# Optimization experiments

Hardware: AMD Instinct MI355X
Metric: run time of the kernel (lower is better)

## Reference

```python
import jax, jax.numpy as jnp
import numpy as np

B, N, K, OUT = 32, 8192, 64, 384
EPS = 1e-5  # BatchNorm eps (torch default)


def setup_inputs() -> dict:
    key = jax.random.key(0)
    ks = jax.random.split(key, 20)
    p = lambda k, shape: jax.random.normal(k, shape, dtype=jnp.float32) * 0.05
    return {
        "normalized_xyz": jax.random.normal(ks[0], (B, N, 3), dtype=jnp.float32),
        "choice": jax.random.randint(ks[1], (B, N), 0, K, dtype=jnp.int32),
        # first_conv: Conv1d(3,128,1) + BN(128) + ReLU + Conv1d(128,256,1)
        "W1": p(ks[2], (128, 3)), "b1": p(ks[3], (128,)),
        "g1": 1.0 + p(ks[4], (128,)), "be1": p(ks[5], (128,)),
        "m1": p(ks[6], (128,)),
        "v1": jax.random.uniform(ks[7], (128,), minval=0.5, maxval=1.5, dtype=jnp.float32),
        "W2": p(ks[8], (256, 128)), "b2": p(ks[9], (256,)),
        # second_conv: Conv1d(512,512,1) + BN(512) + ReLU + Conv1d(512,OUT,1)
        "W3": p(ks[10], (512, 512)), "b3": p(ks[11], (512,)),
        "g2": 1.0 + p(ks[12], (512,)), "be2": p(ks[13], (512,)),
        "m2": p(ks[14], (512,)),
        "v2": jax.random.uniform(ks[15], (512,), minval=0.5, maxval=1.5, dtype=jnp.float32),
        "W4": p(ks[16], (OUT, 512)), "b4": p(ks[17], (OUT,)),
    }


def reference(normalized_xyz, choice, W1, b1, g1, be1, m1, v1, W2, b2,
              W3, b3, g2, be2, m2, v2, W4, b4):
    Bsz, Np, _ = normalized_xyz.shape
    # first_conv: 1x1 convs == per-point matmuls (channel-last layout)
    h = jnp.einsum('bnc,dc->bnd', normalized_xyz, W1) + b1          # [B,N,128]
    h = g1 * (h - m1) / jnp.sqrt(v1 + EPS) + be1                    # BN (eval)
    h = jax.nn.relu(h)
    feat = jnp.einsum('bnd,ed->bne', h, W2) + b2                    # [B,N,256]
    # segmented max over clusters: offset segment ids per batch element
    seg = (choice + jnp.arange(Bsz, dtype=choice.dtype)[:, None] * K).reshape(-1)
    fg = jax.ops.segment_max(feat.reshape(Bsz * Np, -1), seg,
                             num_segments=Bsz * K).reshape(Bsz, K, -1)  # [B,K,256]
    # gather cluster max back to each point
    fg_pts = jnp.take_along_axis(fg, choice[:, :, None], axis=1)   # [B,N,256]
    h = jnp.concatenate([fg_pts, feat], axis=-1)                    # [B,N,512]
    # second_conv
    h = jnp.einsum('bnc,dc->bnd', h, W3) + b3                       # [B,N,512]
    h = g2 * (h - m2) / jnp.sqrt(v2 + EPS) + be2
    h = jax.nn.relu(h)
    feat2 = jnp.einsum('bnd,ed->bne', h, W4) + b4                   # [B,N,OUT]
    out = jax.ops.segment_max(feat2.reshape(Bsz * Np, -1), seg,
                              num_segments=Bsz * K).reshape(Bsz, K, -1)  # [B,K,OUT]
    return out
```

## Files before the change

kernel.cpp:

```cpp
#include <hip/hip_runtime.h>
#include <hip/hip_bf16.h>

#define BB 32
#define NN 8192
#define KK 64
#define OUTC 384
#define EPSB 1e-5f

typedef short bf16x8 __attribute__((ext_vector_type(8)));
typedef float f32x4 __attribute__((ext_vector_type(4)));
typedef unsigned int u32x2 __attribute__((ext_vector_type(2)));
typedef unsigned int u32x4 __attribute__((ext_vector_type(4)));

static __device__ __forceinline__ unsigned short f2b(float x) {
  union { float f; unsigned int u; } v; v.f = x;
  unsigned int r = v.u + 0x7FFFu + ((v.u >> 16) & 1u);
  return (unsigned short)(r >> 16);
}
static __device__ __forceinline__ float b2f(unsigned short h) {
  union { unsigned int u; float f; } v; v.u = ((unsigned int)h) << 16;
  return v.f;
}
static __device__ __forceinline__ unsigned int cvtpk(float lo, float hi) {
  unsigned int r;
  asm("v_cvt_pk_bf16_f32 %0, %1, %2" : "=v"(r) : "v"(lo), "v"(hi));
  return r;
}

__global__ void prep(const float* W1, const float* b1, const float* g1, const float* be1,
                     const float* m1, const float* v1,
                     const float* W2, const float* W3, const float* b3, const float* W4,
                     const float* g2, const float* be2, const float* m2, const float* v2,
                     float* W1f, float* bco,
                     unsigned short* W2b, unsigned short* W3s, unsigned short* W3ls,
                     unsigned short* W4b)
{
  int i = blockIdx.x * blockDim.x + threadIdx.x;
  int T = gridDim.x * blockDim.x;
  for (int d = i; d < 128; d += T) {
    float s1 = g1[d] / sqrtf(v1[d] + EPSB);
    W1f[d*4+0] = s1 * W1[d*3+0];
    W1f[d*4+1] = s1 * W1[d*3+1];
    W1f[d*4+2] = s1 * W1[d*3+2];
    W1f[d*4+3] = s1 * (b1[d] - m1[d]) + be1[d];
  }
  for (int n = i; n < 512; n += T) {
    float s = g2[n] / sqrtf(v2[n] + EPSB);
    bco[n] = s * b3[n] + be2[n] - s * m2[n];
  }
  for (int x = i; x < 256*128; x += T) {
    int c = x >> 7, kk = x & 127;
    int lane = (((kk & 31) >> 3) << 4) | (c & 15);
    int frag = (c >> 4) * 4 + (kk >> 5);
    W2b[frag*512 + lane*8 + (kk & 7)] = f2b(W2[x]);
  }
  for (int x = i; x < 512*256; x += T) {
    int n = x >> 8, kk = x & 255;
    float s = g2[n] / sqrtf(v2[n] + EPSB);
    int lane = (((kk & 31) >> 3) << 4) | (n & 15);
    int frag = (n >> 4) * 8 + (kk >> 5);
    W3s[frag*512 + lane*8 + (kk & 7)] = f2b(s * W3[n*512 + 256 + kk]);
    W3ls[x] = f2b(s * W3[n*512 + kk]);
  }
  for (int x = i; x < 384*512; x += T) {
    int n = x >> 9, kk = x & 511;
    int lane = (((kk & 31) >> 3) << 4) | (n & 15);
    int frag = (n >> 4) * 16 + (kk >> 5);
    W4b[frag*512 + lane*8 + (kk & 7)] = f2b(W4[x]);
  }
}

__global__ void sortk(const int* __restrict__ choice, int* __restrict__ ord,
                      int* __restrict__ seg)
{
  int b = blockIdx.x;
  int t = threadIdx.x;
  __shared__ int hist[KK];
  __shared__ int base[KK];
  if (t < KK) hist[t] = 0;
  __syncthreads();
  for (int i = t; i < NN; i += blockDim.x) atomicAdd(&hist[choice[b*NN + i]], 1);
  __syncthreads();
  if (t == 0) {
    int acc = 0;
    for (int k = 0; k < KK; ++k) { base[k] = acc; seg[b*(KK+1)+k] = acc; acc += hist[k]; }
    seg[b*(KK+1)+KK] = acc;
  }
  __syncthreads();
  for (int i = t; i < NN; i += blockDim.x) {
    int c = choice[b*NN + i];
    int pos = atomicAdd(&base[c], 1);
    ord[b*NN + pos] = i;
  }
}

__global__ __launch_bounds__(256) void k_feat(const float* __restrict__ xyz,
                                              const int* __restrict__ ord,
                                              const float* __restrict__ W1f,
                                              const unsigned short* __restrict__ W2b,
                                              const float* __restrict__ b2,
                                              unsigned short* __restrict__ feat)
{
  __shared__ float lW1[128*4];
  __shared__ __align__(16) char hA[64*256];
  __shared__ __align__(16) char hO[64*512];
  int t = threadIdx.x;
  int b = blockIdx.x >> 7;
  int posbase = (blockIdx.x & 127) * 64;
  if (t < 128) ((f32x4*)lW1)[t] = ((const f32x4*)W1f)[t];
  __syncthreads();

  {
    int r = t >> 2;
    int q = t & 3;
    int p = ord[b*NN + posbase + r];
    const float* xp = xyz + (size_t)(b*NN + p)*3;
    float x0 = xp[0], x1 = xp[1], x2 = xp[2];
#pragma unroll
    for (int dd = 0; dd < 32; dd += 2) {
      int d = q*32 + dd;
      f32x4 w0 = ((const f32x4*)lW1)[d];
      f32x4 w1 = ((const f32x4*)lW1)[d+1];
      float v0 = fmaxf(fmaf(x2, w0[2], fmaf(x1, w0[1], fmaf(x0, w0[0], w0[3]))), 0.0f);
      float v1 = fmaxf(fmaf(x2, w1[2], fmaf(x1, w1[1], fmaf(x0, w1[0], w1[3]))), 0.0f);
      unsigned int pk = cvtpk(v0, v1);
      int byte = ((r*128 + d)*2) ^ ((r & 7) << 4);
      *(unsigned int*)(hA + byte) = pk;
    }
  }
  __syncthreads();

  int lane = t & 63, w = t >> 6;
  int lrow = lane & 15, lhi = lane >> 4;
  f32x4 acc[4][4];
#pragma unroll
  for (int cf = 0; cf < 4; ++cf)
#pragma unroll
    for (int pf = 0; pf < 4; ++pf) acc[cf][pf] = (f32x4)0.0f;

#pragma unroll
  for (int ks = 0; ks < 4; ++ks) {
    int k0 = ks*32 + lhi*8;
    bf16x8 haf[4];
#pragma unroll
    for (int pf = 0; pf < 4; ++pf) {
      int row = pf*16 + lrow;
      int byte = ((row*128 + k0)*2) ^ ((row & 7) << 4);
      haf[pf] = *(const bf16x8*)(hA + byte);
    }
    bf16x8 wf[4];
#pragma unroll
    for (int cf = 0; cf < 4; ++cf) {
      int frag = ((w*4 + cf)*4 + ks);
      wf[cf] = *(const bf16x8*)(W2b + frag*512 + lane*8);
    }
#pragma unroll
    for (int cf = 0; cf < 4; ++cf)
#pragma unroll
      for (int pf = 0; pf < 4; ++pf)
        acc[cf][pf] = __builtin_amdgcn_mfma_f32_16x16x32_bf16(wf[cf], haf[pf], acc[cf][pf], 0, 0, 0);
  }

#pragma unroll
  for (int cf = 0; cf < 4; ++cf) {
    int c0 = w*64 + cf*16 + 4*lhi;
    f32x4 bv = *(const f32x4*)(b2 + c0);
#pragma unroll
    for (int pf = 0; pf < 4; ++pf) {
      int row = pf*16 + lrow;
      u32x2 pk;
      pk[0] = cvtpk(acc[cf][pf][0] + bv[0], acc[cf][pf][1] + bv[1]);
      pk[1] = cvtpk(acc[cf][pf][2] + bv[2], acc[cf][pf][3] + bv[3]);
      int byte = (row*512 + c0*2) ^ ((row & 7) << 4);
      *(u32x2*)(hO + byte) = pk;
    }
  }
  __syncthreads();

#pragma unroll
  for (int cc = 0; cc < 8; ++cc) {
    int lin = w*8192 + cc*1024 + lane*16;
    int row = lin >> 9;
    int off = lin & 511;
    int src = (row*512 + off) ^ ((row & 7) << 4);
    u32x4 v = *(const u32x4*)(hO + src);
    __builtin_nontemporal_store(v,
        (u32x4*)((char*)(feat + (size_t)(b*NN + posbase + row)*256) + off));
  }
}

__global__ __launch_bounds__(256) void k_fg(const unsigned short* __restrict__ feat,
                                            const int* __restrict__ seg,
                                            unsigned short* __restrict__ fg)
{
  __shared__ float red[8][256];
  int blk = blockIdx.x;
  int b = blk >> 6, k = blk & 63;
  int s = seg[b*(KK+1)+k], e = seg[b*(KK+1)+k+1];
  int t = threadIdx.x;
  int rg = t >> 5;
  int cg = t & 31;
  float m[8];
#pragma unroll
  for (int j = 0; j < 8; ++j) m[j] = -1e30f;
  for (int i = s + rg; i < e; i += 8) {
    u32x4 v = __builtin_nontemporal_load(
        (const u32x4*)(feat + (size_t)(b*NN + i)*256 + cg*8));
#pragma unroll
    for (int j = 0; j < 4; ++j) {
      unsigned int u = v[j];
      m[2*j]   = fmaxf(m[2*j],   b2f((unsigned short)(u & 0xffffu)));
      m[2*j+1] = fmaxf(m[2*j+1], b2f((unsigned short)(u >> 16)));
    }
  }
#pragma unroll
  for (int j = 0; j < 8; ++j) red[rg][cg*8 + j] = m[j];
  __syncthreads();
  float mm = red[0][t];
#pragma unroll
  for (int j = 1; j < 8; ++j) mm = fmaxf(mm, red[j][t]);
  fg[(b*KK + k)*256 + t] = f2b(mm);
}

__global__ __launch_bounds__(256) void k_dv(const unsigned short* __restrict__ fg,
                                            const unsigned short* __restrict__ W3ls,
                                            const float* __restrict__ bco,
                                            float* __restrict__ Dv)
{
  __shared__ __align__(16) char As[32*512];
  int t = threadIdx.x;
  int row0 = blockIdx.x * 32;
  {
    int r = t >> 3;
    const char* src = (const char*)(fg + (size_t)(row0 + r)*256);
    int cbase = (t & 7) * 16;
#pragma unroll
    for (int cc = 0; cc < 4; ++cc) {
      int byteoff = cbase + cc*128;
      int dst = (r*512 + byteoff) ^ ((r & 7) << 4);
      *(u32x4*)(As + dst) = *(const u32x4*)(src + byteoff);
    }
  }
  __syncthreads();

  int lane = t & 63, w = t >> 6;
  int lrow = lane & 15, lhi = lane >> 4;

  f32x4 acc[2][8];
#pragma unroll
  for (int m = 0; m < 2; ++m)
#pragma unroll
    for (int nt = 0; nt < 8; ++nt) acc[m][nt] = (f32x4)0.0f;

#pragma unroll 2
  for (int ks = 0; ks < 8; ++ks) {
    int koff = ks*32 + lhi*8;
    bf16x8 af[2];
#pragma unroll
    for (int m = 0; m < 2; ++m) {
      int row = m*16 + lrow;
      int byte = (row*512 + koff*2) ^ ((row & 7) << 4);
      af[m] = *(const bf16x8*)(As + byte);
    }
    bf16x8 bf[8];
#pragma unroll
    for (int nt = 0; nt < 8; ++nt) {
      int n = w*128 + nt*16 + lrow;
      bf[nt] = *(const bf16x8*)(W3ls + n*256 + koff);
    }
#pragma unroll
    for (int m = 0; m < 2; ++m)
#pragma unroll
      for (int nt = 0; nt < 8; ++nt)
        acc[m][nt] = __builtin_amdgcn_mfma_f32_16x16x32_bf16(af[m], bf[nt], acc[m][nt], 0, 0, 0);
  }

#pragma unroll
  for (int m = 0; m < 2; ++m)
#pragma unroll
    for (int nt = 0; nt < 8; ++nt) {
      int n = w*128 + nt*16 + lrow;
      float bc = bco[n];
#pragma unroll
      for (int rr = 0; rr < 4; ++rr) {
        int row = m*16 + lhi*4 + rr;
        Dv[(size_t)(row0 + row)*512 + n] = acc[m][nt][rr] + bc;
      }
    }
}

__global__ __launch_bounds__(512, 2) void k_out(const unsigned short* __restrict__ feat,
                                                const int* __restrict__ seg,
                                                const float* __restrict__ Dv,
                                                const unsigned short* __restrict__ W3s,
                                                const unsigned short* __restrict__ W4b,
                                                const float* __restrict__ b4,
                                                float* __restrict__ out)
{
  __shared__ float Dvs[512];
  __shared__ float rm[OUTC];
  __shared__ __align__(16) char As[48*512];
  __shared__ __align__(16) char Mid[48*512];
  int blk = blockIdx.x;
  int b = blk >> 6, k = blk & 63;
  int t = threadIdx.x;
  int s = seg[b*(KK+1)+k], e = seg[b*(KK+1)+k+1];
  int S = e - s;

  Dvs[t] = Dv[(size_t)(b*KK + k)*512 + t];
  if (t < OUTC) rm[t] = -1e30f;

  int lane = t & 63, w = t >> 6;
  int lrow = lane & 15, lhi = lane >> 4;

  int lim = b*NN + NN - 1;
  int srow[3], sdst[3], soff[3];
#pragma unroll
  for (int j = 0; j < 3; ++j) {
    int c = t + j*512;
    srow[j] = c >> 5;
    soff[j] = (c & 31) * 16;
    sdst[j] = (srow[j]*512 + soff[j]) ^ ((srow[j] & 7) << 4);
  }

#pragma unroll
  for (int j = 0; j < 3; ++j) {
    int pos = b*NN + s + srow[j];
    if (pos > lim) pos = lim;
    const char* src = (const char*)(feat + (size_t)pos*256);
    u32x4 v = __builtin_nontemporal_load((const u32x4*)(src + soff[j]));
    *(u32x4*)(As + sdst[j]) = v;
  }

  for (int mt = 0; mt < S; mt += 48) {
    __syncthreads();

    bool do_stage = (mt + 48 < S);
    u32x4 sv[3];
    f32x4 acc4[3][3];
#pragma unroll
    for (int m = 0; m < 3; ++m)
#pragma unroll
      for (int nt = 0; nt < 3; ++nt) acc4[m][nt] = (f32x4)0.0f;

#pragma unroll 1
    for (int h = 0; h < 2; ++h) {
      {
        f32x4 acc2[2][3];
#pragma unroll
        for (int nf = 0; nf < 2; ++nf)
#pragma unroll
          for (int pf = 0; pf < 3; ++pf) acc2[nf][pf] = (f32x4)0.0f;

#pragma unroll 2
        for (int ks = 0; ks < 8; ++ks) {
          int koff = ks*32 + lhi*8;
          bf16x8 asf[3];
#pragma unroll
          for (int pf = 0; pf < 3; ++pf) {
            int row = pf*16 + lrow;
            int byte = (row*512 + koff*2) ^ ((row & 7) << 4);
            asf[pf] = *(const bf16x8*)(As + byte);
          }
          bf16x8 w3f[2];
#pragma unroll
          for (int nf = 0; nf < 2; ++nf) {
            int frag = (h*16 + w*2 + nf)*8 + ks;
            w3f[nf] = *(const bf16x8*)(W3s + frag*512 + lane*8);
          }
          __builtin_amdgcn_s_setprio(1);
#pragma unroll
          for (int nf = 0; nf < 2; ++nf)
#pragma unroll
            for (int pf = 0; pf < 3; ++pf)
              acc2[nf][pf] = __builtin_amdgcn_mfma_f32_16x16x32_bf16(w3f[nf], asf[pf], acc2[nf][pf], 0, 0, 0);
          __builtin_amdgcn_s_setprio(0);
        }

#pragma unroll
        for (int nf = 0; nf < 2; ++nf) {
          int nl0 = w*32 + nf*16 + 4*lhi;
          f32x4 d4 = *(const f32x4*)(Dvs + h*256 + nl0);
#pragma unroll
          for (int pf = 0; pf < 3; ++pf) {
            int row = pf*16 + lrow;
            float v0 = fmaxf(acc2[nf][pf][0] + d4[0], 0.0f);
            float v1 = fmaxf(acc2[nf][pf][1] + d4[1], 0.0f);
            float v2 = fmaxf(acc2[nf][pf][2] + d4[2], 0.0f);
            float v3 = fmaxf(acc2[nf][pf][3] + d4[3], 0.0f);
            u32x2 pk;
            pk[0] = cvtpk(v0, v1);
            pk[1] = cvtpk(v2, v3);
            int byte = (row*512 + nl0*2) ^ ((row & 7) << 4);
            *(u32x2*)(Mid + byte) = pk;
          }
        }
      }
      __syncthreads();

      if (h == 0 && do_stage) {
#pragma unroll
        for (int j = 0; j < 3; ++j) {
          int pos = b*NN + s + mt + 48 + srow[j];
          if (pos > lim) pos = lim;
          const char* src = (const char*)(feat + (size_t)pos*256);
          sv[j] = __builtin_nontemporal_load((const u32x4*)(src + soff[j]));
        }
      }

#pragma unroll 2
      for (int ks = 0; ks < 8; ++ks) {
        int koff = ks*32 + lhi*8;
        bf16x8 af[3];
#pragma unroll
        for (int m = 0; m < 3; ++m) {
          int row = m*16 + lrow;
          int byte = (row*512 + koff*2) ^ ((row & 7) << 4);
          af[m] = *(const bf16x8*)(Mid + byte);
        }
        bf16x8 bf[3];
#pragma unroll
        for (int nt = 0; nt < 3; ++nt) {
          int frag = (w*3 + nt)*16 + h*8 + ks;
          bf[nt] = *(const bf16x8*)(W4b + frag*512 + lane*8);
        }
        __builtin_amdgcn_s_setprio(1);
#pragma unroll
        for (int m = 0; m < 3; ++m)
#pragma unroll
          for (int nt = 0; nt < 3; ++nt)
            acc4[m][nt] = __builtin_amdgcn_mfma_f32_16x16x32_bf16(af[m], bf[nt], acc4[m][nt], 0, 0, 0);
        __builtin_amdgcn_s_setprio(0);
      }

      if (h == 0) __syncthreads();
    }

    if (do_stage) {
#pragma unroll
      for (int j = 0; j < 3; ++j) *(u32x4*)(As + sdst[j]) = sv[j];
    }

#pragma unroll
    for (int nt = 0; nt < 3; ++nt) {
      float v = -1e30f;
#pragma unroll
      for (int m = 0; m < 3; ++m)
#pragma unroll
        for (int rr = 0; rr < 4; ++rr) {
          int rowg = mt + m*16 + lhi*4 + rr;
          v = (rowg < S) ? fmaxf(v, acc4[m][nt][rr]) : v;
        }
      v = fmaxf(v, __shfl_xor(v, 16, 64));
      v = fmaxf(v, __shfl_xor(v, 32, 64));
      if (lane < 16) {
        int col = w*48 + nt*16 + lrow;
        rm[col] = fmaxf(rm[col], v);
      }
    }
  }
  __syncthreads();

  if (t < OUTC) out[(b*KK + k)*OUTC + t] = rm[t] + b4[t];
}

extern "C" void kernel_launch(void* const* d_in, const int* in_sizes, int n_in,
                              void* d_out, int out_size, void* d_ws, size_t ws_size,
                              hipStream_t stream)
{
  const float* xyz   = (const float*)d_in[0];
  const int*   choice= (const int*)  d_in[1];
  const float* W1    = (const float*)d_in[2];
  const float* b1    = (const float*)d_in[3];
  const float* g1    = (const float*)d_in[4];
  const float* be1   = (const float*)d_in[5];
  const float* m1    = (const float*)d_in[6];
  const float* v1    = (const float*)d_in[7];
  const float* W2    = (const float*)d_in[8];
  const float* b2    = (const float*)d_in[9];
  const float* W3    = (const float*)d_in[10];
  const float* b3    = (const float*)d_in[11];
  const float* g2    = (const float*)d_in[12];
  const float* be2   = (const float*)d_in[13];
  const float* m2    = (const float*)d_in[14];
  const float* v2    = (const float*)d_in[15];
  const float* W4    = (const float*)d_in[16];
  const float* b4    = (const float*)d_in[17];

  char* ws = (char*)d_ws;
  size_t o = 0;
  int* ord             = (int*)(ws + o);            o += (size_t)BB*NN*4;
  int* seg             = (int*)(ws + o);            o += 64*1024;
  float* W1f           = (float*)(ws + o);          o += 4*1024;
  float* bco           = (float*)(ws + o);          o += 4*1024;
  unsigned short* W2b  = (unsigned short*)(ws + o); o += (size_t)256*128*2;
  unsigned short* W3s  = (unsigned short*)(ws + o); o += (size_t)512*256*2;
  unsigned short* W3ls = (unsigned short*)(ws + o); o += (size_t)512*256*2;
  unsigned short* W4b  = (unsigned short*)(ws + o); o += (size_t)384*512*2;
  unsigned short* fg   = (unsigned short*)(ws + o); o += (size_t)BB*KK*256*2;
  float* Dv            = (float*)(ws + o);          o += (size_t)BB*KK*512*4;
  unsigned short* feat = (unsigned short*)(ws + o); o += (size_t)BB*NN*256*2;

  prep<<<512, 256, 0, stream>>>(W1, b1, g1, be1, m1, v1, W2, W3, b3, W4,
                                g2, be2, m2, v2, W1f, bco, W2b, W3s, W3ls, W4b);
  sortk<<<BB, 256, 0, stream>>>(choice, ord, seg);
  k_feat<<<BB*NN/64, 256, 0, stream>>>(xyz, ord, W1f, W2b, b2, feat);
  k_fg<<<BB*KK, 256, 0, stream>>>(feat, seg, fg);
  k_dv<<<BB*KK/32, 256, 0, stream>>>(fg, W3ls, bco, Dv);
  k_out<<<BB*KK, 512, 0, stream>>>(feat, seg, Dv, W3s, W4b, b4, (float*)d_out);
}
```

Baseline: 352.4 us.

## Restructure k_out to compute full 512-wide mid tile once, raise occupancy

Instead of splitting the second-conv hidden dimension into two halves, each followed by a partial W4 GEMM, the kernel now computes all 512 mid channels into a doubled shared buffer and then runs a single 16-step W4 GEMM. The next tile's feat prefetch becomes a direct global-to-LDS store placed between the phases, which drops the register-held prefetch. Launch bounds are raised from 2 to 8 waves per SIMD and the loops are not unrolled, to cut register pressure and raise occupancy. The cost is twice the shared memory for Mid, which may cap resident blocks, and less overlap of global loads with MFMA work.

Measured after the change: 319.0 us. 9.5% less time.

```diff
diff --git a/kernel.cpp b/kernel.cpp
--- a/kernel.cpp
+++ b/kernel.cpp
@@ -289,7 +289,7 @@
     }
 }
 
-__global__ __launch_bounds__(512, 2) void k_out(const unsigned short* __restrict__ feat,
+__global__ __launch_bounds__(512, 8) void k_out(const unsigned short* __restrict__ feat,
                                                 const int* __restrict__ seg,
                                                 const float* __restrict__ Dv,
                                                 const unsigned short* __restrict__ W3s,
@@ -300,7 +300,7 @@
   __shared__ float Dvs[512];
   __shared__ float rm[OUTC];
   __shared__ __align__(16) char As[48*512];
-  __shared__ __align__(16) char Mid[48*512];
+  __shared__ __align__(16) char Mid[48*1024];
   int blk = blockIdx.x;
   int b = blk >> 6, k = blk & 63;
   int t = threadIdx.x;
@@ -335,127 +335,116 @@
   for (int mt = 0; mt < S; mt += 48) {
     __syncthreads();
 
-    bool do_stage = (mt + 48 < S);
-    u32x4 sv[3];
-    f32x4 acc4[3][3];
-#pragma unroll
-    for (int m = 0; m < 3; ++m)
-#pragma unroll
-      for (int nt = 0; nt < 3; ++nt) acc4[m][nt] = (f32x4)0.0f;
-
 #pragma unroll 1
-    for (int h = 0; h < 2; ++h) {
-      {
-        f32x4 acc2[2][3];
+    for (int g = 0; g < 2; ++g) {
+      f32x4 acc2[2][3];
+#pragma unroll
+      for (int nf = 0; nf < 2; ++nf)
+#pragma unroll
+        for (int pf = 0; pf < 3; ++pf) acc2[nf][pf] = (f32x4)0.0f;
+
+#pragma unroll 1
+      for (int ks = 0; ks < 8; ++ks) {
+        int koff = ks*32 + lhi*8;
+        bf16x8 asf[3];
+#pragma unroll
+        for (int pf = 0; pf < 3; ++pf) {
+          int row = pf*16 + lrow;
+          int byte = (row*512 + koff*2) ^ ((row & 7) << 4);
+          asf[pf] = *(const bf16x8*)(As + byte);
+        }
+        bf16x8 w3f[2];
+#pragma unroll
+        for (int nf = 0; nf < 2; ++nf) {
+          int frag = (w*4 + g*2 + nf)*8 + ks;
+          w3f[nf] = *(const bf16x8*)(W3s + frag*512 + lane*8);
+        }
+        __builtin_amdgcn_s_setprio(1);
 #pragma unroll
         for (int nf = 0; nf < 2; ++nf)
 #pragma unroll
-          for (int pf = 0; pf < 3; ++pf) acc2[nf][pf] = (f32x4)0.0f;
-
-#pragma unroll 2
-        for (int ks = 0; ks < 8; ++ks) {
-          int koff = ks*32 + lhi*8;
-          bf16x8 asf[3];
-#pragma unroll
-          for (int pf = 0; pf < 3; ++pf) {
-            int row = pf*16 + lrow;
-            int byte = (row*512 + koff*2) ^ ((row & 7) << 4);
-            asf[pf] = *(const bf16x8*)(As + byte);
-          }
-          bf16x8 w3f[2];
-#pragma unroll
-          for (int nf = 0; nf < 2; ++nf) {
-            int frag = (h*16 + w*2 + nf)*8 + ks;
-            w3f[nf] = *(const bf16x8*)(W3s + frag*512 + lane*8);
-          }
-          __builtin_amdgcn_s_setprio(1);
-#pragma unroll
-          for (int nf = 0; nf < 2; ++nf)
-#pragma unroll
-            for (int pf = 0; pf < 3; ++pf)
-              acc2[nf][pf] = __builtin_amdgcn_mfma_f32_16x16x32_bf16(w3f[nf], asf[pf], acc2[nf][pf], 0, 0, 0);
-          __builtin_amdgcn_s_setprio(0);
-        }
-
-#pragma unroll
-        for (int nf = 0; nf < 2; ++nf) {
-          int nl0 = w*32 + nf*16 + 4*lhi;
-          f32x4 d4 = *(const f32x4*)(Dvs + h*256 + nl0);
-#pragma unroll
-          for (int pf = 0; pf < 3; ++pf) {
-            int row = pf*16 + lrow;
-            float v0 = fmaxf(acc2[nf][pf][0] + d4[0], 0.0f);
-            float v1 = fmaxf(acc2[nf][pf][1] + d4[1], 0.0f);
-            float v2 = fmaxf(acc2[nf][pf][2] + d4[2], 0.0f);
-            float v3 = fmaxf(acc2[nf][pf][3] + d4[3], 0.0f);
-            u32x2 pk;
-            pk[0] = cvtpk(v0, v1);
-            pk[1] = cvtpk(v2, v3);
-            int byte = (row*512 + nl0*2) ^ ((row & 7) << 4);
-            *(u32x2*)(Mid + byte) = pk;
-          }
+          for (int pf = 0; pf < 3; ++pf)
+            acc2[nf][pf] = __builtin_amdgcn_mfma_f32_16x16x32_bf16(w3f[nf], asf[pf], acc2[nf][pf], 0, 0, 0);
+        __builtin_amdgcn_s_setprio(0);
+      }
+
+#pragma unroll
+      for (int nf = 0; nf < 2; ++nf) {
+        int n0 = w*64 + (g*2 + nf)*16 + 4*lhi;
+        f32x4 d4 = *(const f32x4*)(Dvs + n0);
+#pragma unroll
+        for (int pf = 0; pf < 3; ++pf) {
+          int row = pf*16 + lrow;
+          float v0 = fmaxf(acc2[nf][pf][0] + d4[0], 0.0f);
+          float v1 = fmaxf(acc2[nf][pf][1] + d4[1], 0.0f);
+          float v2 = fmaxf(acc2[nf][pf][2] + d4[2], 0.0f);
+          float v3 = fmaxf(acc2[nf][pf][3] + d4[3], 0.0f);
+          u32x2 pk;
+          pk[0] = cvtpk(v0, v1);
+          pk[1] = cvtpk(v2, v3);
+          int byte = (row*1024 + n0*2) ^ ((row & 7) << 4);
+          *(u32x2*)(Mid + byte) = pk;
         }
       }
-      __syncthreads();
-
-      if (h == 0 && do_stage) {
-#pragma unroll
-        for (int j = 0; j < 3; ++j) {
-          int pos = b*NN + s + mt + 48 + srow[j];
-          if (pos > lim) pos = lim;
-          const char* src = (const char*)(feat + (size_t)pos*256);
-          sv[j] = __builtin_nontemporal_load((const u32x4*)(src + soff[j]));
-        }
+    }
+    __syncthreads();
+
+    if (mt + 48 < S) {
+#pragma unroll
+      for (int j = 0; j < 3; ++j) {
+        int pos = b*NN + s + mt + 48 + srow[j];
+        if (pos > lim) pos = lim;
+        const char* src = (const char*)(feat + (size_t)pos*256);
+        u32x4 v = __builtin_nontemporal_load((const u32x4*)(src + soff[j]));
+        *(u32x4*)(As + sdst[j]) = v;
       }
-
-#pragma unroll 2
-      for (int ks = 0; ks < 8; ++ks) {
+    }
+
+    {
+      f32x4 acc4[3][3];
+#pragma unroll
+      for (int m = 0; m < 3; ++m)
+#pragma unroll
+        for (int nt = 0; nt < 3; ++nt) acc4[m][nt] = (f32x4)0.0f;
+
+#pragma unroll 1
+      for (int ks = 0; ks < 16; ++ks) {
         int koff = ks*32 + lhi*8;
         bf16x8 af[3];
 #pragma unroll
         for (int m = 0; m < 3; ++m) {
           int row = m*16 + lrow;
-          int byte = (row*512 + koff*2) ^ ((row & 7) << 4);
+          int byte = (row*1024 + koff*2) ^ ((row & 7) << 4);
           af[m] = *(const bf16x8*)(Mid + byte);
         }
-        bf16x8 bf[3];
+        __builtin_amdgcn_s_setprio(1);
 #pragma unroll
         for (int nt = 0; nt < 3; ++nt) {
-          int frag = (w*3 + nt)*16 + h*8 + ks;
-          bf[nt] = *(const bf16x8*)(W4b + frag*512 + lane*8);
+          int frag = (w*3 + nt)*16 + ks;
+          bf16x8 bf = *(const bf16x8*)(W4b + frag*512 + lane*8);
+#pragma unroll
+          for (int m = 0; m < 3; ++m)
+            acc4[m][nt] = __builtin_amdgcn_mfma_f32_16x16x32_bf16(af[m], bf, acc4[m][nt], 0, 0, 0);
         }
-        __builtin_amdgcn_s_setprio(1);
-#pragma unroll
-        for (int m = 0; m < 3; ++m)
-#pragma unroll
-          for (int nt = 0; nt < 3; ++nt)
-            acc4[m][nt] = __builtin_amdgcn_mfma_f32_16x16x32_bf16(af[m], bf[nt], acc4[m][nt], 0, 0, 0);
         __builtin_amdgcn_s_setprio(0);
       }
 
-      if (h == 0) __syncthreads();
-    }
-
-    if (do_stage) {
-#pragma unroll
-      for (int j = 0; j < 3; ++j) *(u32x4*)(As + sdst[j]) = sv[j];
-    }
-
-#pragma unroll
-    for (int nt = 0; nt < 3; ++nt) {
-      float v = -1e30f;
-#pragma unroll
-      for (int m = 0; m < 3; ++m)
-#pragma unroll
-        for (int rr = 0; rr < 4; ++rr) {
-          int rowg = mt + m*16 + lhi*4 + rr;
-          v = (rowg < S) ? fmaxf(v, acc4[m][nt][rr]) : v;
+#pragma unroll
+      for (int nt = 0; nt < 3; ++nt) {
+        float v = -1e30f;
+#pragma unroll
+        for (int m = 0; m < 3; ++m)
+#pragma unroll
+          for (int rr = 0; rr < 4; ++rr) {
+            int rowg = mt + m*16 + lhi*4 + rr;
+            v = (rowg < S) ? fmaxf(v, acc4[m][nt][rr]) : v;
+          }
+        v = fmaxf(v, __shfl_xor(v, 16, 64));
+        v = fmaxf(v, __shfl_xor(v, 32, 64));
+        if (lane < 16) {
+          int col = w*48 + nt*16 + lrow;
+          rm[col] = fmaxf(rm[col], v);
         }
-      v = fmaxf(v, __shfl_xor(v, 16, 64));
-      v = fmaxf(v, __shfl_xor(v, 32, 64));
-      if (lane < 16) {
-        int col = w*48 + nt*16 + lrow;
-        rm[col] = fmaxf(rm[col], v);
       }
     }
   }
```
